# Optimization experiments

Hardware: AMD Instinct MI355X
Metric: run time of the kernel (lower is better)

## Reference

```python
import jax, jax.numpy as jnp
import numpy as np

EPS = 1e-10


def setup_inputs() -> dict:
    key = jax.random.key(0)
    kx, ky = jax.random.split(key)
    x = jax.random.normal(kx, (8, 8192, 3), dtype=jnp.float32)
    y = jax.random.normal(ky, (8, 8192, 3), dtype=jnp.float32)
    return {"x": x, "y": y}


def reference(x, y):
    # x: (B, N, 3), y: (B, M, 3)
    xy = -2.0 * jnp.einsum("bnd,bmd->bnm", x, y)          # (B, N, M)
    xx = jnp.sum(x * x, axis=-1, keepdims=True)            # (B, N, 1)
    yy = jnp.sum(y * y, axis=-1, keepdims=True)            # (B, M, 1)
    dist = jnp.sqrt(xy + xx + jnp.swapaxes(yy, 1, 2) + EPS)  # (B, N, M)
    distance1 = jnp.min(dist, axis=2)                      # (B, N): x -> nearest y
    distance2 = jnp.min(dist, axis=1)                      # (B, M): y -> nearest x
    mean1 = jnp.mean(distance1, axis=-1)                   # (B,)
    mean2 = jnp.mean(distance2, axis=-1)                   # (B,)
    return jnp.sum(jnp.maximum(mean1, mean2))
```

## Files before the change

### kernel.cpp

```cpp
#include <hip/hip_runtime.h>


#define BB 8
#define NN 8192
#define NPTS (BB*NN)
#define BLK 256
#define CCOLS 256
#define CT 8
#define RT 4
#define STRIPS 16

typedef __attribute__((ext_vector_type(8))) short bf16x8;
typedef __attribute__((ext_vector_type(16))) float f32x16;

__device__ __forceinline__ unsigned f2mono(float f) {
    unsigned u = __float_as_uint(f);
    return u ^ ((unsigned)((int)u >> 31) | 0x80000000u);
}
__device__ __forceinline__ float mono2f(unsigned m) {
    unsigned u = ((int)m >= 0) ? ~m : (m ^ 0x80000000u);
    return __uint_as_float(u);
}
__device__ __forceinline__ unsigned bfh(float v) {
    unsigned u = __float_as_uint(v);
    u += 0x7FFFu + ((u >> 16) & 1u);
    return u >> 16;
}
__device__ __forceinline__ float bff(unsigned h) {
    return __uint_as_float(h << 16);
}
__device__ __forceinline__ unsigned pk(unsigned lo, unsigned hi) {
    return (lo & 0xFFFFu) | (hi << 16);
}

__global__ void prep_kernel(const float* __restrict__ x, const float* __restrict__ y,
                            uint4* __restrict__ afr, uint4* __restrict__ bfr,
                            unsigned* __restrict__ counter) {
    int i = blockIdx.x * BLK + threadIdx.x;
    if (i == 0) *counter = 0;
    const float* src = (i < NPTS) ? x : y;
    int j = (i < NPTS) ? i : i - NPTS;
    float c0 = src[3*j], c1 = src[3*j+1], c2 = src[3*j+2];
    float s2 = c0*c0 + c1*c1 + c2*c2;
    unsigned sh = bfh(s2), sl = bfh(s2 - bff(sh));
    float a0 = -2.f*c0, a1 = -2.f*c1, a2 = -2.f*c2;
    unsigned ah0 = bfh(a0), ah1 = bfh(a1), ah2 = bfh(a2);
    unsigned al0 = bfh(a0 - bff(ah0)), al1 = bfh(a1 - bff(ah1)), al2 = bfh(a2 - bff(ah2));
    unsigned bh0 = bfh(c0), bh1 = bfh(c1), bh2 = bfh(c2);
    unsigned bl0 = bfh(c0 - bff(bh0)), bl1 = bfh(c1 - bff(bh1)), bl2 = bfh(c2 - bff(bh2));
    const unsigned one = 0x3F80u;
    afr[2*i]   = make_uint4(pk(ah0,ah1), pk(ah2,al0), pk(al1,al2), pk(ah0,ah1));
    afr[2*i+1] = make_uint4(pk(ah2,sh),  pk(sl,one),  pk(one,0u),  0u);
    bfr[2*i]   = make_uint4(pk(bh0,bh1), pk(bh2,bh0), pk(bh1,bh2), pk(bl0,bl1));
    bfr[2*i+1] = make_uint4(pk(bl2,one), pk(one,sh),  pk(sl,0u),   0u);
}

__device__ __forceinline__ bf16x8 cvt(uint4 v) { return __builtin_bit_cast(bf16x8, v); }

__global__ __launch_bounds__(BLK, 2) void
main_kernel(const uint4* __restrict__ afr, const uint4* __restrict__ bfr,
            float* __restrict__ bpart, unsigned* __restrict__ counter,
            float* __restrict__ out) {
    __shared__ unsigned colmin[CCOLS];
    __shared__ float red[4];
    __shared__ float gg[8];
    __shared__ int lastflag;
    const int bi  = blockIdx.x;
    const int dir = bi >> 8;
    const int b   = (bi >> 5) & 7;
    const int cc  = bi & 31;
    const uint4* Af = afr + (dir ? 2*NPTS : 0);
    const uint4* Bf = bfr + (dir ? 0 : 2*NPTS);
    const int tid = threadIdx.x;
    const int lane = tid & 63, w = tid >> 6;
    const int m = lane & 31;
    const int hb = lane >> 5;

    colmin[tid] = 0xFFFFFFFFu;

    bf16x8 bf[CT];
#pragma unroll
    for (int ct = 0; ct < CT; ++ct) {
        int c = b * NN + cc * CCOLS + ct * 32 + m;
        bf[ct] = cvt(Bf[2*c + hb]);
    }

    f32x16 zro;
#pragma unroll
    for (int i = 0; i < 16; ++i) zro[i] = 0.f;

    float rm[CT];
#pragma unroll
    for (int ct = 0; ct < CT; ++ct) rm[ct] = 3.4e38f;

    const int rowbase = b * NN + w * 128 + m;
    uint4 cur[RT], nxt[RT];
#pragma unroll
    for (int t = 0; t < RT; ++t) cur[t] = Af[2*(rowbase + t*32) + hb];

#pragma unroll 1
    for (int s = 0; s < STRIPS; ++s) {
        const int np = (s + 1 < STRIPS) ? (s + 1) : s;
#pragma unroll
        for (int t = 0; t < RT; ++t) nxt[t] = Af[2*(rowbase + np*512 + t*32) + hb];
#pragma unroll
        for (int ct = 0; ct < CT; ++ct) {
            f32x16 a0 = __builtin_amdgcn_mfma_f32_32x32x16_bf16(cvt(cur[0]), bf[ct], zro, 0, 0, 0);
            f32x16 a1 = __builtin_amdgcn_mfma_f32_32x32x16_bf16(cvt(cur[1]), bf[ct], zro, 0, 0, 0);
            f32x16 a2 = __builtin_amdgcn_mfma_f32_32x32x16_bf16(cvt(cur[2]), bf[ct], zro, 0, 0, 0);
            f32x16 a3 = __builtin_amdgcn_mfma_f32_32x32x16_bf16(cvt(cur[3]), bf[ct], zro, 0, 0, 0);
            float p = rm[ct];
#pragma unroll
            for (int r = 0; r < 16; ++r) {
                float t0 = fminf(fminf(a0[r], a1[r]), a2[r]);
                p = fminf(fminf(t0, a3[r]), p);
            }
            rm[ct] = p;
        }
#pragma unroll
        for (int t = 0; t < RT; ++t) cur[t] = nxt[t];
    }

#pragma unroll
    for (int ct = 0; ct < CT; ++ct) {
        float p = fminf(rm[ct], __shfl_xor(rm[ct], 32, 64));
        if (hb == 0) atomicMin(&colmin[ct * 32 + m], f2mono(p));
    }
    __syncthreads();

    float d = sqrtf(fmaxf(mono2f(colmin[tid]), 0.f) + 1e-10f);
#pragma unroll
    for (int off = 32; off; off >>= 1) d += __shfl_down(d, off, 64);
    if (lane == 0) red[w] = d;
    __syncthreads();
    if (tid == 0) {
        float total = red[0] + red[1] + red[2] + red[3];
        atomicExch(&bpart[bi], total);
        __threadfence();
        unsigned old = atomicAdd(counter, 1u);
        lastflag = (old == 511u);
    }
    __syncthreads();

    if (lastflag) {
        float v0 = atomicAdd(&bpart[tid], 0.f);
        float v1 = atomicAdd(&bpart[256 + tid], 0.f);
#pragma unroll
        for (int off = 16; off; off >>= 1) {
            v0 += __shfl_down(v0, off, 32);
            v1 += __shfl_down(v1, off, 32);
        }
        if ((tid & 31) == 0) gg[tid >> 5] = fmaxf(v0, v1);
        __syncthreads();
        if (tid == 0) {
            float acc = 0.f;
#pragma unroll
            for (int k = 0; k < 8; ++k) acc += gg[k];
            out[0] = acc * (1.0f / (float)NN);
        }
    }
}

extern "C" void kernel_launch(void* const* d_in, const int* in_sizes, int n_in,
                              void* d_out, int out_size, void* d_ws, size_t ws_size,
                              hipStream_t stream) {
    const float* x = (const float*)d_in[0];
    const float* y = (const float*)d_in[1];
    float* out = (float*)d_out;

    char* ws = (char*)d_ws;
    uint4* afr = (uint4*)ws;
    uint4* bfr = afr + 4 * NPTS;
    float* bpart = (float*)(bfr + 4 * NPTS);
    unsigned* counter = (unsigned*)(bpart + 512);

    prep_kernel<<<(2 * NPTS) / BLK, BLK, 0, stream>>>(x, y, afr, bfr, counter);
    main_kernel<<<512, BLK, 0, stream>>>(afr, bfr, bpart, counter, out);
}
```

Measured before the change: 100.2 us.

## Halve per-block tile to double grid and occupancy, split min-reduction chains

Each block now covers 128 columns instead of 256, and each wave processes 2 row tiles per strip instead of 4. This doubles the grid to 1024 blocks and raises the launch-bounds occupancy target from 2 to 4. The row-min reduction is split into four independent fmin chains to cut dependency latency. The final cross-block reduction is adapted to the larger grid. Smaller tiles mean less B-fragment reuse per A load, so row fragments are fetched more often in exchange for more waves hiding latency.

```diff
diff --git a/kernel.cpp b/kernel.cpp
--- a/kernel.cpp
+++ b/kernel.cpp
@@ -5,10 +5,11 @@
 #define NN 8192
 #define NPTS (BB*NN)
 #define BLK 256
-#define CCOLS 256
-#define CT 8
-#define RT 4
-#define STRIPS 16
+#define CCOLS 128
+#define CT 4
+#define RT 2
+#define STRIPS 32
+#define GRID 1024
 
 typedef __attribute__((ext_vector_type(8))) short bf16x8;
 typedef __attribute__((ext_vector_type(16))) float f32x16;
@@ -57,7 +58,7 @@
 
 __device__ __forceinline__ bf16x8 cvt(uint4 v) { return __builtin_bit_cast(bf16x8, v); }
 
-__global__ __launch_bounds__(BLK, 2) void
+__global__ __launch_bounds__(BLK, 4) void
 main_kernel(const uint4* __restrict__ afr, const uint4* __restrict__ bfr,
             float* __restrict__ bpart, unsigned* __restrict__ counter,
             float* __restrict__ out) {
@@ -66,9 +67,9 @@
     __shared__ float gg[8];
     __shared__ int lastflag;
     const int bi  = blockIdx.x;
-    const int dir = bi >> 8;
-    const int b   = (bi >> 5) & 7;
-    const int cc  = bi & 31;
+    const int dir = bi >> 9;
+    const int b   = (bi >> 6) & 7;
+    const int cc  = bi & 63;
     const uint4* Af = afr + (dir ? 2*NPTS : 0);
     const uint4* Bf = bfr + (dir ? 0 : 2*NPTS);
     const int tid = threadIdx.x;
@@ -76,7 +77,7 @@
     const int m = lane & 31;
     const int hb = lane >> 5;
 
-    colmin[tid] = 0xFFFFFFFFu;
+    if (tid < CCOLS) colmin[tid] = 0xFFFFFFFFu;
 
     bf16x8 bf[CT];
 #pragma unroll
@@ -93,7 +94,7 @@
 #pragma unroll
     for (int ct = 0; ct < CT; ++ct) rm[ct] = 3.4e38f;
 
-    const int rowbase = b * NN + w * 128 + m;
+    const int rowbase = b * NN + w * 64 + m;
     uint4 cur[RT], nxt[RT];
 #pragma unroll
     for (int t = 0; t < RT; ++t) cur[t] = Af[2*(rowbase + t*32) + hb];
@@ -102,20 +103,24 @@
     for (int s = 0; s < STRIPS; ++s) {
         const int np = (s + 1 < STRIPS) ? (s + 1) : s;
 #pragma unroll
-        for (int t = 0; t < RT; ++t) nxt[t] = Af[2*(rowbase + np*512 + t*32) + hb];
+        for (int t = 0; t < RT; ++t) nxt[t] = Af[2*(rowbase + np*256 + t*32) + hb];
+        bf16x8 ca = cvt(cur[0]), cb = cvt(cur[1]);
 #pragma unroll
         for (int ct = 0; ct < CT; ++ct) {
-            f32x16 a0 = __builtin_amdgcn_mfma_f32_32x32x16_bf16(cvt(cur[0]), bf[ct], zro, 0, 0, 0);
-            f32x16 a1 = __builtin_amdgcn_mfma_f32_32x32x16_bf16(cvt(cur[1]), bf[ct], zro, 0, 0, 0);
-            f32x16 a2 = __builtin_amdgcn_mfma_f32_32x32x16_bf16(cvt(cur[2]), bf[ct], zro, 0, 0, 0);
-            f32x16 a3 = __builtin_amdgcn_mfma_f32_32x32x16_bf16(cvt(cur[3]), bf[ct], zro, 0, 0, 0);
-            float p = rm[ct];
+            f32x16 a0 = __builtin_amdgcn_mfma_f32_32x32x16_bf16(ca, bf[ct], zro, 0, 0, 0);
+            f32x16 a1 = __builtin_amdgcn_mfma_f32_32x32x16_bf16(cb, bf[ct], zro, 0, 0, 0);
+            float m0 = fminf(fminf(a0[0], a1[0]), rm[ct]);
+            float m1 = fminf(a0[1], a1[1]);
+            float m2 = fminf(a0[2], a1[2]);
+            float m3 = fminf(a0[3], a1[3]);
 #pragma unroll
-            for (int r = 0; r < 16; ++r) {
-                float t0 = fminf(fminf(a0[r], a1[r]), a2[r]);
-                p = fminf(fminf(t0, a3[r]), p);
+            for (int r = 4; r < 16; r += 4) {
+                m0 = fminf(fminf(a0[r],   a1[r]),   m0);
+                m1 = fminf(fminf(a0[r+1], a1[r+1]), m1);
+                m2 = fminf(fminf(a0[r+2], a1[r+2]), m2);
+                m3 = fminf(fminf(a0[r+3], a1[r+3]), m3);
             }
-            rm[ct] = p;
+            rm[ct] = fminf(fminf(m0, m1), fminf(m2, m3));
         }
 #pragma unroll
         for (int t = 0; t < RT; ++t) cur[t] = nxt[t];
@@ -128,7 +133,7 @@
     }
     __syncthreads();
 
-    float d = sqrtf(fmaxf(mono2f(colmin[tid]), 0.f) + 1e-10f);
+    float d = (tid < CCOLS) ? sqrtf(fmaxf(mono2f(colmin[tid]), 0.f) + 1e-10f) : 0.f;
 #pragma unroll
     for (int off = 32; off; off >>= 1) d += __shfl_down(d, off, 64);
     if (lane == 0) red[w] = d;
@@ -138,13 +143,13 @@
         atomicExch(&bpart[bi], total);
         __threadfence();
         unsigned old = atomicAdd(counter, 1u);
-        lastflag = (old == 511u);
+        lastflag = (old == (GRID - 1));
     }
     __syncthreads();
 
     if (lastflag) {
-        float v0 = atomicAdd(&bpart[tid], 0.f);
-        float v1 = atomicAdd(&bpart[256 + tid], 0.f);
+        float v0 = atomicAdd(&bpart[2*tid], 0.f) + atomicAdd(&bpart[2*tid+1], 0.f);
+        float v1 = atomicAdd(&bpart[512 + 2*tid], 0.f) + atomicAdd(&bpart[512 + 2*tid+1], 0.f);
 #pragma unroll
         for (int off = 16; off; off >>= 1) {
             v0 += __shfl_down(v0, off, 32);
@@ -172,8 +177,8 @@
     uint4* afr = (uint4*)ws;
     uint4* bfr = afr + 4 * NPTS;
     float* bpart = (float*)(bfr + 4 * NPTS);
-    unsigned* counter = (unsigned*)(bpart + 512);
+    unsigned* counter = (unsigned*)(bpart + GRID);
 
     prep_kernel<<<(2 * NPTS) / BLK, BLK, 0, stream>>>(x, y, afr, bfr, counter);
-    main_kernel<<<512, BLK, 0, stream>>>(afr, bfr, bpart, counter, out);
+    main_kernel<<<GRID, BLK, 0, stream>>>(afr, bfr, bpart, counter, out);
 }
```

After: 117.6 us. 17.3% more time.

## Software-pipeline MFMA issue with min3 reduction using inline asm and sched barriers

Applied to the files above, without the earlier changes.

Halves the row tile per wave (RT 4->2, STRIPS 16->32) and hand-schedules the inner loop. MFMAs for the next column tile are issued via inline asm while the previous tile's results are reduced with v_min3_f32. Double-buffered accumulators and sched barriers enforce this interleaving, aiming to hide MFMA latency behind VALU min reductions and cut the VALU instruction count. It risks compiler-inserted hazard waits around the asm MFMA outputs and less row reuse of each B fragment per strip.

```diff
diff --git a/kernel.cpp b/kernel.cpp
--- a/kernel.cpp
+++ b/kernel.cpp
@@ -7,8 +7,8 @@
 #define BLK 256
 #define CCOLS 256
 #define CT 8
-#define RT 4
-#define STRIPS 16
+#define RT 2
+#define STRIPS 32
 
 typedef __attribute__((ext_vector_type(8))) short bf16x8;
 typedef __attribute__((ext_vector_type(16))) float f32x16;
@@ -57,6 +57,40 @@
 
 __device__ __forceinline__ bf16x8 cvt(uint4 v) { return __builtin_bit_cast(bf16x8, v); }
 
+#define SB() __builtin_amdgcn_sched_barrier(0)
+
+#define MFMA_V(D, A, B)                                                        \
+    asm("v_mfma_f32_32x32x16_bf16 %0, %1, %2, %3"                              \
+        : "=&v"(D) : "v"(A), "v"(B), "v"(zro))
+
+#define MIN3(d, a, b, c)                                                       \
+    asm("v_min3_f32 %0, %1, %2, %3" : "=v"(d) : "v"(a), "v"(b), "v"(c))
+
+#define ISSUE2(B, R0, R1)                                                      \
+    MFMA_V(R0, ca0, (B));                                                      \
+    MFMA_V(R1, ca1, (B));
+
+#define RED2(P0, P1, RM) do {                                                  \
+    float g0_, g1_, g2_, g3_, g4_, g5_, g6_, g7_, g8_, g9_, g10_;              \
+    float h0_, h1_, h2_, u0_;                                                  \
+    MIN3(g0_,  P0[0],  P0[1],  P0[2]);                                         \
+    MIN3(g1_,  P0[3],  P0[4],  P0[5]);                                         \
+    MIN3(g2_,  P0[6],  P0[7],  P0[8]);                                         \
+    MIN3(g3_,  P0[9],  P0[10], P0[11]);                                        \
+    MIN3(g4_,  P0[12], P0[13], P0[14]);                                        \
+    MIN3(g5_,  P0[15], P1[0],  P1[1]);                                         \
+    MIN3(g6_,  P1[2],  P1[3],  P1[4]);                                         \
+    MIN3(g7_,  P1[5],  P1[6],  P1[7]);                                         \
+    MIN3(g8_,  P1[8],  P1[9],  P1[10]);                                        \
+    MIN3(g9_,  P1[11], P1[12], P1[13]);                                        \
+    MIN3(g10_, P1[14], P1[15], (RM));                                          \
+    MIN3(h0_, g0_, g1_, g2_);                                                  \
+    MIN3(h1_, g3_, g4_, g5_);                                                  \
+    MIN3(h2_, g6_, g7_, g8_);                                                  \
+    MIN3(u0_, h0_, h1_, h2_);                                                  \
+    MIN3((RM), u0_, g9_, g10_);                                                \
+} while (0)
+
 __global__ __launch_bounds__(BLK, 2) void
 main_kernel(const uint4* __restrict__ afr, const uint4* __restrict__ bfr,
             float* __restrict__ bpart, unsigned* __restrict__ counter,
@@ -93,7 +127,7 @@
 #pragma unroll
     for (int ct = 0; ct < CT; ++ct) rm[ct] = 3.4e38f;
 
-    const int rowbase = b * NN + w * 128 + m;
+    const int rowbase = b * NN + w * 64 + m;
     uint4 cur[RT], nxt[RT];
 #pragma unroll
     for (int t = 0; t < RT; ++t) cur[t] = Af[2*(rowbase + t*32) + hb];
@@ -102,21 +136,29 @@
     for (int s = 0; s < STRIPS; ++s) {
         const int np = (s + 1 < STRIPS) ? (s + 1) : s;
 #pragma unroll
-        for (int t = 0; t < RT; ++t) nxt[t] = Af[2*(rowbase + np*512 + t*32) + hb];
-#pragma unroll
-        for (int ct = 0; ct < CT; ++ct) {
-            f32x16 a0 = __builtin_amdgcn_mfma_f32_32x32x16_bf16(cvt(cur[0]), bf[ct], zro, 0, 0, 0);
-            f32x16 a1 = __builtin_amdgcn_mfma_f32_32x32x16_bf16(cvt(cur[1]), bf[ct], zro, 0, 0, 0);
-            f32x16 a2 = __builtin_amdgcn_mfma_f32_32x32x16_bf16(cvt(cur[2]), bf[ct], zro, 0, 0, 0);
-            f32x16 a3 = __builtin_amdgcn_mfma_f32_32x32x16_bf16(cvt(cur[3]), bf[ct], zro, 0, 0, 0);
-            float p = rm[ct];
-#pragma unroll
-            for (int r = 0; r < 16; ++r) {
-                float t0 = fminf(fminf(a0[r], a1[r]), a2[r]);
-                p = fminf(fminf(t0, a3[r]), p);
-            }
-            rm[ct] = p;
-        }
+        for (int t = 0; t < RT; ++t) nxt[t] = Af[2*(rowbase + np*256 + t*32) + hb];
+
+        const bf16x8 ca0 = cvt(cur[0]), ca1 = cvt(cur[1]);
+
+        f32x16 e0, e1, o0, o1;
+        ISSUE2(bf[0], e0, e1);
+        ISSUE2(bf[1], o0, o1);
+        SB();
+        RED2(e0, e1, rm[0]);  ISSUE2(bf[2], e0, e1);
+        SB();
+        RED2(o0, o1, rm[1]);  ISSUE2(bf[3], o0, o1);
+        SB();
+        RED2(e0, e1, rm[2]);  ISSUE2(bf[4], e0, e1);
+        SB();
+        RED2(o0, o1, rm[3]);  ISSUE2(bf[5], o0, o1);
+        SB();
+        RED2(e0, e1, rm[4]);  ISSUE2(bf[6], e0, e1);
+        SB();
+        RED2(o0, o1, rm[5]);  ISSUE2(bf[7], o0, o1);
+        SB();
+        RED2(e0, e1, rm[6]);
+        RED2(o0, o1, rm[7]);
+
 #pragma unroll
         for (int t = 0; t < RT; ++t) cur[t] = nxt[t];
     }
```

Measured after the change: 97.88 us. 1.02x faster.
